# Kernel optimization log

Measured on AMD Instinct MI355X. Metric: run time of the kernel, lower is better.

The kernel has to match this reference:

```python
import jax, jax.numpy as jnp
import numpy as np

K_CENTERS = 128   # SA K
RADIUS = 1.0      # SA r
D = 3             # spatial dim (module-level d)
IFD = 64          # input feature dim
L1, L2, L3 = 64, 64, 128
N_POINTS = 8192


def setup_inputs() -> dict:
    key = jax.random.key(0)
    ks = jax.random.split(key, 8)
    coords = jax.random.normal(ks[0], (N_POINTS, D), dtype=jnp.float32)
    features = jax.random.normal(ks[1], (N_POINTS, IFD), dtype=jnp.float32)

    def lin(kw, kb, fan_in, fan_out):
        bound = 1.0 / np.sqrt(fan_in)
        W = jax.random.uniform(kw, (fan_in, fan_out), jnp.float32, -bound, bound)
        b = jax.random.uniform(kb, (fan_out,), jnp.float32, -bound, bound)
        return W, b

    W1, b1 = lin(ks[2], ks[3], D + IFD, L1)
    W2, b2 = lin(ks[4], ks[5], L1, L2)
    W3, b3 = lin(ks[6], ks[7], L2, L3)
    return dict(coords=coords, features=features,
                W1=W1, b1=b1, W2=W2, b2=b2, W3=W3, b3=b3)


def farthest_point_sample(coords, k):
    """Iterative FPS starting from point 0 (pytorch3d default). Returns [k] indices."""
    n = coords.shape[0]

    def step(carry, _):
        dists, last = carry
        d2 = jnp.sum((coords - coords[last]) ** 2, axis=1)  # [N]
        dists = jnp.minimum(dists, d2)
        nxt = jnp.argmax(dists).astype(jnp.int32)
        return (dists, nxt), nxt

    init = (jnp.full((n,), 1e10, coords.dtype), jnp.int32(0))
    (_, _), rest = jax.lax.scan(step, init, None, length=k - 1)
    return jnp.concatenate([jnp.zeros((1,), jnp.int32), rest])


def reference(coords, features, W1, b1, W2, b2, W3, b3):
    # 1) Farthest point sampling -> K centers
    idx = farthest_point_sample(coords, K_CENTERS)
    centers = coords[idx]                                  # [K, 3]

    # 2) Ball-query grouping (mask form): point p in group(c) iff ||p - c|| < r.
    rel = coords[None, :, :] - centers[:, None, :]         # [K, N, 3] (coords - center)
    mask = jnp.linalg.norm(rel, axis=-1) < RADIUS          # [K, N]

    # 3) Per-group PointNet: shared MLP on [rel_coords, features], then masked max over group.
    feat = jnp.broadcast_to(features[None, :, :], (K_CENTERS,) + features.shape)
    x = jnp.concatenate([rel, feat], axis=-1)              # [K, N, 3+ifd]
    h = jax.nn.relu(x @ W1 + b1)                           # [K, N, l1]
    h = jax.nn.relu(h @ W2 + b2)                           # [K, N, l2]
    h = jax.nn.relu(h @ W3 + b3)                           # [K, N, l3]
    h = jnp.where(mask[..., None], h, -jnp.inf)            # exclude out-of-ball points
    out_features = jnp.max(h, axis=1)                      # [K, l3]
    return centers, out_features
```

## Files before the change

kernel.cpp:

```cpp
#include <hip/hip_runtime.h>

#define N_POINTS 8192
#define K_CENTERS 128
#define IFD 64
#define L1D 64
#define L2D 64
#define L3D 128
#define QS 4096

#define LD4(p) (*(const float4*)(p))

template <int CTRL, int RMASK>
__device__ __forceinline__ void dpp_max_u64(unsigned& hi, unsigned& lo) {
  unsigned h2 = (unsigned)__builtin_amdgcn_update_dpp(
      (int)hi, (int)hi, CTRL, RMASK, 0xF, false);
  unsigned l2 = (unsigned)__builtin_amdgcn_update_dpp(
      (int)lo, (int)lo, CTRL, RMASK, 0xF, false);
  unsigned long long a = ((unsigned long long)hi << 32) | lo;
  unsigned long long b = ((unsigned long long)h2 << 32) | l2;
  if (b > a) { hi = h2; lo = l2; }
}

#define FPS_T 512
#define FPS_P (N_POINTS / FPS_T)

#define SMEM_BYTES (98304 + 128)

__global__ __launch_bounds__(FPS_T) void fps_gt_kernel(
    const float* __restrict__ coords, float* __restrict__ out_centers,
    const float* __restrict__ features, const float* __restrict__ W1,
    const float* __restrict__ b1, float* __restrict__ GT,
    int* __restrict__ counts, float* __restrict__ out_feat) {
  __shared__ __align__(16) char smem[SMEM_BYTES];
  const int tid = threadIdx.x;

  if (blockIdx.x != 0) {
    float* w = (float*)smem;
    const int bk = blockIdx.x - 1;
    if (bk == 0 && tid < K_CENTERS) counts[tid] = 0;
    if (bk == 1) {
#pragma unroll 1
      for (int s = tid; s < K_CENTERS * L3D; s += FPS_T) out_feat[s] = 0.0f;
    }
    const int n0 = bk * 64;
    for (int s = tid; s < IFD * L1D; s += FPS_T) w[s] = W1[3 * L1D + s];
    __syncthreads();
    const int j = tid & 63;
    const int nl = tid >> 6;
    const float bj = b1[j];
#pragma unroll 1
    for (int itn = 0; itn < 8; itn++) {
      const int nn = nl + itn * 8;
      const float* __restrict__ frow = features + (size_t)(n0 + nn) * IFD;
      float acc = bj;
#pragma unroll 16
      for (int i = 0; i < IFD; i++) acc = fmaf(frow[i], w[i * 64 + j], acc);
      GT[(size_t)(n0 + nn) * 64 + j] = acc;
    }
    return;
  }

  float* clds = (float*)smem;
  unsigned long long* wmax = (unsigned long long*)(smem + 98304);
  const int lane = tid & 63;
  const int wid = tid >> 6;

  {
    const float4* __restrict__ src = (const float4*)coords;
    float4* dst = (float4*)smem;
#pragma unroll
    for (int i = 0; i < 12; i++) dst[tid + i * FPS_T] = src[tid + i * FPS_T];
  }

  float px[FPS_P], py[FPS_P], pz[FPS_P], mind[FPS_P];
#pragma unroll
  for (int i = 0; i < FPS_P; i++) {
    int n = tid + i * FPS_T;
    px[i] = coords[3 * n];
    py[i] = coords[3 * n + 1];
    pz[i] = coords[3 * n + 2];
    mind[i] = 1e10f;
  }

  float cx = coords[0], cy = coords[1], cz = coords[2];
  if (tid == 0) {
    out_centers[0] = cx; out_centers[1] = cy; out_centers[2] = cz;
  }
  __syncthreads();

  for (int it = 1; it < K_CENTERS; it++) {
#pragma unroll
    for (int i = 0; i < FPS_P; i++) {
      float dx = px[i] - cx, dy = py[i] - cy, dz = pz[i] - cz;
      float d2 = dx * dx + dy * dy + dz * dz;
      mind[i] = fminf(mind[i], d2);
    }
    float t8[8];
#pragma unroll
    for (int i = 0; i < 8; i++) t8[i] = fmaxf(mind[i], mind[i + 8]);
#pragma unroll
    for (int i = 0; i < 4; i++) t8[i] = fmaxf(t8[i], t8[i + 4]);
    const float bm = fmaxf(fmaxf(t8[0], t8[1]), fmaxf(t8[2], t8[3]));
    int cand[FPS_P];
#pragma unroll
    for (int i = 0; i < FPS_P; i++)
      cand[i] = (mind[i] == bm) ? (tid + i * FPS_T) : 0x7FFFFFFF;
#pragma unroll
    for (int s = 8; s > 0; s >>= 1)
#pragma unroll
      for (int i = 0; i < s; i++) cand[i] = min(cand[i], cand[i + s]);

    unsigned hi = __float_as_uint(bm);
    unsigned lo = (unsigned)(N_POINTS - 1 - cand[0]);
    dpp_max_u64<0xB1, 0xF>(hi, lo);
    dpp_max_u64<0x4E, 0xF>(hi, lo);
    dpp_max_u64<0x141, 0xF>(hi, lo);
    dpp_max_u64<0x140, 0xF>(hi, lo);
    dpp_max_u64<0x142, 0xA>(hi, lo);
    dpp_max_u64<0x143, 0xC>(hi, lo);
    const int buf = it & 1;
    if (lane == 63)
      wmax[(buf << 3) + wid] = ((unsigned long long)hi << 32) | lo;
    __syncthreads();

    const unsigned long long* __restrict__ wb = wmax + (buf << 3);
    unsigned long long a0 = wb[0], a1 = wb[1], a2 = wb[2], a3 = wb[3];
    unsigned long long a4 = wb[4], a5 = wb[5], a6 = wb[6], a7 = wb[7];
    a0 = a0 > a4 ? a0 : a4;
    a1 = a1 > a5 ? a1 : a5;
    a2 = a2 > a6 ? a2 : a6;
    a3 = a3 > a7 ? a3 : a7;
    a0 = a0 > a2 ? a0 : a2;
    a1 = a1 > a3 ? a1 : a3;
    a0 = a0 > a1 ? a0 : a1;
    const int widx = N_POINTS - 1 - (int)(a0 & 0xFFFFFFFFull);
    cx = clds[widx * 3];
    cy = clds[widx * 3 + 1];
    cz = clds[widx * 3 + 2];
    if (tid == 0) {
      out_centers[3 * it] = cx;
      out_centers[3 * it + 1] = cy;
      out_centers[3 * it + 2] = cz;
    }
  }
}

#define PREP_PARTS 4
#define PREP_PTS (N_POINTS / PREP_PARTS)

__global__ __launch_bounds__(256) void prep_kernel(
    const float* __restrict__ coords, const float* __restrict__ centers,
    int* __restrict__ counts, int* __restrict__ Q) {
  const int tid = threadIdx.x;
  const int k = blockIdx.x >> 2;
  const int part = blockIdx.x & 3;
  const float cx = centers[3 * k], cy = centers[3 * k + 1],
              cz = centers[3 * k + 2];
  const int nbase = part * PREP_PTS;
#pragma unroll
  for (int s = 0; s < PREP_PTS / 256; s++) {
    const int n = nbase + s * 256 + tid;
    float dx = coords[3 * n] - cx;
    float dy = coords[3 * n + 1] - cy;
    float dz = coords[3 * n + 2] - cz;
    float d2 = dx * dx + dy * dy + dz * dz;
    if (sqrtf(d2) < 1.0f) {
      int p = atomicAdd(&counts[k], 1);
      if (p < QS) Q[(k << 12) + p] = n;
    }
  }
}

#define MLP_BLOCKS 1024

__global__ __launch_bounds__(256, 4) void mlp_kernel(
    const float* __restrict__ coords, const float* __restrict__ GT,
    const float* __restrict__ W1, const float* __restrict__ W2,
    const float* __restrict__ b2, const float* __restrict__ W3,
    const float* __restrict__ b3, const float* __restrict__ centers,
    const int* __restrict__ counts, const int* __restrict__ Q,
    float* __restrict__ out_feat) {
  __shared__ float gt2[64 * 65];
  __shared__ float cst[3 * 64 + 64 + 128];
  const int tid = threadIdx.x;
  const int lane = tid & 63;
  const int wid = tid >> 6;
  const int gu = __builtin_amdgcn_readfirstlane(wid);

  for (int s = tid; s < 384; s += 256) {
    float v;
    if (s < 192) v = W1[s];
    else if (s < 256) v = b2[s - 192];
    else v = b3[s - 256];
    cst[s] = v;
  }

  int c0c = counts[lane];      if (c0c > QS) c0c = QS;
  int c1c = counts[64 + lane]; if (c1c > QS) c1c = QS;
  int s0 = (c0c + 63) >> 6;
  int s1 = (c1c + 63) >> 6;
#pragma unroll
  for (int off = 1; off < 64; off <<= 1) {
    int t0 = __shfl_up(s0, off, 64);
    int t1 = __shfl_up(s1, off, 64);
    if (lane >= off) { s0 += t0; s1 += t1; }
  }
  s1 += __shfl(s0, 63, 64);
  const int C = __shfl(s1, 63, 64);
  const int p1 = s0;
  const int p65 = s1;

  const int cpb = (C + MLP_BLOCKS - 1) / MLP_BLOCKS;
  const int cbeg = blockIdx.x * cpb;
  const int cend = min(cbeg + cpb, C);
  __syncthreads();
  if (cbeg >= C) return;

  float vmax[32];
#pragma unroll
  for (int t = 0; t < 32; t++) vmax[t] = 0.0f;
  int kprev = -1;

  for (int c = cbeg; c < cend; c++) {
    int k = __popcll(__ballot(p1 <= c)) + __popcll(__ballot(p65 <= c));
    k = __builtin_amdgcn_readfirstlane(k);
    int pk = 0;
    if (k > 0)
      pk = (k <= 64) ? __shfl(s0, k - 1, 64) : __shfl(s1, k - 65, 64);
    int Mk = counts[k];
    if (Mk > QS) Mk = QS;
    const int m0 = (c - pk) * 64;
    const int base = (k << 12) + m0;
    const int mcap = Mk - 1 - m0;

    if (k != kprev) {
      if (kprev >= 0) {
#pragma unroll
        for (int t = 0; t < 32; t++) {
          float v = vmax[t];
#pragma unroll
          for (int off = 32; off >= 1; off >>= 1)
            v = fmaxf(v, __shfl_xor(v, off, 64));
          if (lane == 0)
            atomicMax((unsigned int*)&out_feat[kprev * L3D + gu * 32 + t],
                      __float_as_uint(v));
          vmax[t] = 0.0f;
        }
      }
      kprev = k;
    }

#pragma unroll 4
    for (int it = 0; it < 16; it++) {
      int row = (gu << 4) + it;
      int rr = row < mcap ? row : mcap;
      int nrow = Q[base + rr];
      nrow = __builtin_amdgcn_readfirstlane(nrow);
      gt2[row * 65 + lane] = GT[(size_t)nrow * 64 + lane];
    }
    __syncthreads();

    int m = m0 + lane;
    if (m >= Mk) m = Mk - 1;
    const int n = Q[(k << 12) + m];
    const float cx = centers[3 * k], cy = centers[3 * k + 1],
                cz = centers[3 * k + 2];
    const float dx = coords[3 * n] - cx;
    const float dy = coords[3 * n + 1] - cy;
    const float dz = coords[3 * n + 2] - cz;

    float acc[16];
#pragma unroll
    for (int t = 0; t < 16; t++) acc[t] = cst[192 + gu * 16 + t];
    const float* __restrict__ w2u = W2 + gu * 16;
#pragma unroll 4
    for (int i = 0; i < 64; i++) {
      const float g = gt2[lane * 65 + i];
      const float e = fmaxf(
          fmaf(dz, cst[128 + i], fmaf(dy, cst[64 + i], fmaf(dx, cst[i], g))),
          0.0f);
      const float* __restrict__ wr = w2u + i * 64;
#pragma unroll
      for (int t = 0; t < 16; t += 4) {
        const float4 w = LD4(wr + t);
        acc[t + 0] = fmaf(e, w.x, acc[t + 0]);
        acc[t + 1] = fmaf(e, w.y, acc[t + 1]);
        acc[t + 2] = fmaf(e, w.z, acc[t + 2]);
        acc[t + 3] = fmaf(e, w.w, acc[t + 3]);
      }
    }
    __syncthreads();

#pragma unroll
    for (int t = 0; t < 16; t++)
      gt2[lane * 65 + gu * 16 + t] = fmaxf(acc[t], 0.0f);
    __syncthreads();

    float a3[32];
#pragma unroll
    for (int t = 0; t < 32; t++) a3[t] = cst[256 + gu * 32 + t];
    const float* __restrict__ w3u = W3 + gu * 32;
#pragma unroll 2
    for (int i = 0; i < 64; i++) {
      const float hv = gt2[lane * 65 + i];
      const float* __restrict__ wr = w3u + i * L3D;
#pragma unroll
      for (int t = 0; t < 32; t += 4) {
        const float4 w = LD4(wr + t);
        a3[t + 0] = fmaf(hv, w.x, a3[t + 0]);
        a3[t + 1] = fmaf(hv, w.y, a3[t + 1]);
        a3[t + 2] = fmaf(hv, w.z, a3[t + 2]);
        a3[t + 3] = fmaf(hv, w.w, a3[t + 3]);
      }
    }
#pragma unroll
    for (int t = 0; t < 32; t++)
      vmax[t] = fmaxf(vmax[t], fmaxf(a3[t], 0.0f));
    __syncthreads();
  }

#pragma unroll
  for (int t = 0; t < 32; t++) {
    float v = vmax[t];
#pragma unroll
    for (int off = 32; off >= 1; off >>= 1)
      v = fmaxf(v, __shfl_xor(v, off, 64));
    if (lane == 0)
      atomicMax((unsigned int*)&out_feat[kprev * L3D + gu * 32 + t],
                __float_as_uint(v));
  }
}

extern "C" void kernel_launch(void* const* d_in, const int* in_sizes, int n_in,
                              void* d_out, int out_size, void* d_ws,
                              size_t ws_size, hipStream_t stream) {
  const float* coords = (const float*)d_in[0];
  const float* features = (const float*)d_in[1];
  const float* W1 = (const float*)d_in[2];
  const float* b1 = (const float*)d_in[3];
  const float* W2 = (const float*)d_in[4];
  const float* b2 = (const float*)d_in[5];
  const float* W3 = (const float*)d_in[6];
  const float* b3 = (const float*)d_in[7];

  float* out = (float*)d_out;
  float* centers = out;
  float* out_feat = out + K_CENTERS * 3;

  char* ws = (char*)d_ws;
  float* GT = (float*)ws;
  int* Q = (int*)(ws + (size_t)N_POINTS * L1D * 4);
  int* counts = (int*)(ws + 4 * 1024 * 1024);

  fps_gt_kernel<<<1 + K_CENTERS, FPS_T, 0, stream>>>(
      coords, centers, features, W1, b1, GT, counts, out_feat);
  prep_kernel<<<PREP_PARTS * K_CENTERS, 256, 0, stream>>>(coords, centers,
                                                          counts, Q);
  mlp_kernel<<<MLP_BLOCKS, 256, 0, stream>>>(coords, GT, W1, W2, b2, W3, b3,
                                             centers, counts, Q, out_feat);
}
```

Before: 236.3 us.

## Fuse FPS, ball query and MLP into one persistent kernel with flag-based streaming

Merges the three kernels into one persistent launch. Block 0 runs farthest point sampling and publishes each center through a progress counter. The other 160 worker blocks first compute the GT projection, then take (center, slice) tickets and do the ball query and MLP for each center as soon as it is published. This overlaps the serial FPS with the grouping and MLP work and removes the global queue and extra launches. Weights are staged in LDS. The design depends on all blocks being co-resident and on spin-waiting, and the workers may simply stall behind the sequential FPS chain.

```diff
diff --git a/kernel.cpp b/kernel.cpp
--- a/kernel.cpp
+++ b/kernel.cpp
@@ -6,7 +6,6 @@
 #define L1D 64
 #define L2D 64
 #define L3D 128
-#define QS 4096
 
 #define LD4(p) (*(const float4*)(p))
 
@@ -23,311 +22,322 @@
 
 #define FPS_T 512
 #define FPS_P (N_POINTS / FPS_T)
-
 #define SMEM_BYTES (98304 + 128)
 
-__global__ __launch_bounds__(FPS_T) void fps_gt_kernel(
+#define NWORK 160
+#define GT_ROWS 52
+#define SLICES 8
+#define SLICE_PTS (N_POINTS / SLICES)
+#define TICKETS (K_CENTERS * SLICES)
+
+__global__ void zero_ctrl(int* __restrict__ ctrl) {
+  if (threadIdx.x < 8) ctrl[threadIdx.x] = 0;
+}
+
+__global__ __launch_bounds__(512) void fused_kernel(
     const float* __restrict__ coords, float* __restrict__ out_centers,
     const float* __restrict__ features, const float* __restrict__ W1,
-    const float* __restrict__ b1, float* __restrict__ GT,
-    int* __restrict__ counts, float* __restrict__ out_feat) {
+    const float* __restrict__ b1, const float* __restrict__ W2,
+    const float* __restrict__ b2, const float* __restrict__ W3,
+    const float* __restrict__ b3, float* __restrict__ GT,
+    int* __restrict__ ctrl, unsigned* __restrict__ cbuf,
+    float* __restrict__ out_feat) {
   __shared__ __align__(16) char smem[SMEM_BYTES];
-  const int tid = threadIdx.x;
-
-  if (blockIdx.x != 0) {
-    float* w = (float*)smem;
-    const int bk = blockIdx.x - 1;
-    if (bk == 0 && tid < K_CENTERS) counts[tid] = 0;
-    if (bk == 1) {
-#pragma unroll 1
-      for (int s = tid; s < K_CENTERS * L3D; s += FPS_T) out_feat[s] = 0.0f;
-    }
-    const int n0 = bk * 64;
-    for (int s = tid; s < IFD * L1D; s += FPS_T) w[s] = W1[3 * L1D + s];
-    __syncthreads();
-    const int j = tid & 63;
-    const int nl = tid >> 6;
-    const float bj = b1[j];
-#pragma unroll 1
-    for (int itn = 0; itn < 8; itn++) {
-      const int nn = nl + itn * 8;
-      const float* __restrict__ frow = features + (size_t)(n0 + nn) * IFD;
-      float acc = bj;
-#pragma unroll 16
-      for (int i = 0; i < IFD; i++) acc = fmaf(frow[i], w[i * 64 + j], acc);
-      GT[(size_t)(n0 + nn) * 64 + j] = acc;
-    }
-    return;
-  }
-
-  float* clds = (float*)smem;
-  unsigned long long* wmax = (unsigned long long*)(smem + 98304);
-  const int lane = tid & 63;
-  const int wid = tid >> 6;
-
-  {
-    const float4* __restrict__ src = (const float4*)coords;
-    float4* dst = (float4*)smem;
-#pragma unroll
-    for (int i = 0; i < 12; i++) dst[tid + i * FPS_T] = src[tid + i * FPS_T];
-  }
-
-  float px[FPS_P], py[FPS_P], pz[FPS_P], mind[FPS_P];
-#pragma unroll
-  for (int i = 0; i < FPS_P; i++) {
-    int n = tid + i * FPS_T;
-    px[i] = coords[3 * n];
-    py[i] = coords[3 * n + 1];
-    pz[i] = coords[3 * n + 2];
-    mind[i] = 1e10f;
-  }
-
-  float cx = coords[0], cy = coords[1], cz = coords[2];
-  if (tid == 0) {
-    out_centers[0] = cx; out_centers[1] = cy; out_centers[2] = cz;
-  }
-  __syncthreads();
-
-  for (int it = 1; it < K_CENTERS; it++) {
-#pragma unroll
-    for (int i = 0; i < FPS_P; i++) {
-      float dx = px[i] - cx, dy = py[i] - cy, dz = pz[i] - cz;
-      float d2 = dx * dx + dy * dy + dz * dz;
-      mind[i] = fminf(mind[i], d2);
-    }
-    float t8[8];
-#pragma unroll
-    for (int i = 0; i < 8; i++) t8[i] = fmaxf(mind[i], mind[i + 8]);
-#pragma unroll
-    for (int i = 0; i < 4; i++) t8[i] = fmaxf(t8[i], t8[i + 4]);
-    const float bm = fmaxf(fmaxf(t8[0], t8[1]), fmaxf(t8[2], t8[3]));
-    int cand[FPS_P];
-#pragma unroll
-    for (int i = 0; i < FPS_P; i++)
-      cand[i] = (mind[i] == bm) ? (tid + i * FPS_T) : 0x7FFFFFFF;
-#pragma unroll
-    for (int s = 8; s > 0; s >>= 1)
-#pragma unroll
-      for (int i = 0; i < s; i++) cand[i] = min(cand[i], cand[i + s]);
-
-    unsigned hi = __float_as_uint(bm);
-    unsigned lo = (unsigned)(N_POINTS - 1 - cand[0]);
-    dpp_max_u64<0xB1, 0xF>(hi, lo);
-    dpp_max_u64<0x4E, 0xF>(hi, lo);
-    dpp_max_u64<0x141, 0xF>(hi, lo);
-    dpp_max_u64<0x140, 0xF>(hi, lo);
-    dpp_max_u64<0x142, 0xA>(hi, lo);
-    dpp_max_u64<0x143, 0xC>(hi, lo);
-    const int buf = it & 1;
-    if (lane == 63)
-      wmax[(buf << 3) + wid] = ((unsigned long long)hi << 32) | lo;
-    __syncthreads();
-
-    const unsigned long long* __restrict__ wb = wmax + (buf << 3);
-    unsigned long long a0 = wb[0], a1 = wb[1], a2 = wb[2], a3 = wb[3];
-    unsigned long long a4 = wb[4], a5 = wb[5], a6 = wb[6], a7 = wb[7];
-    a0 = a0 > a4 ? a0 : a4;
-    a1 = a1 > a5 ? a1 : a5;
-    a2 = a2 > a6 ? a2 : a6;
-    a3 = a3 > a7 ? a3 : a7;
-    a0 = a0 > a2 ? a0 : a2;
-    a1 = a1 > a3 ? a1 : a3;
-    a0 = a0 > a1 ? a0 : a1;
-    const int widx = N_POINTS - 1 - (int)(a0 & 0xFFFFFFFFull);
-    cx = clds[widx * 3];
-    cy = clds[widx * 3 + 1];
-    cz = clds[widx * 3 + 2];
-    if (tid == 0) {
-      out_centers[3 * it] = cx;
-      out_centers[3 * it + 1] = cy;
-      out_centers[3 * it + 2] = cz;
-    }
-  }
-}
-
-#define PREP_PARTS 4
-#define PREP_PTS (N_POINTS / PREP_PARTS)
-
-__global__ __launch_bounds__(256) void prep_kernel(
-    const float* __restrict__ coords, const float* __restrict__ centers,
-    int* __restrict__ counts, int* __restrict__ Q) {
-  const int tid = threadIdx.x;
-  const int k = blockIdx.x >> 2;
-  const int part = blockIdx.x & 3;
-  const float cx = centers[3 * k], cy = centers[3 * k + 1],
-              cz = centers[3 * k + 2];
-  const int nbase = part * PREP_PTS;
-#pragma unroll
-  for (int s = 0; s < PREP_PTS / 256; s++) {
-    const int n = nbase + s * 256 + tid;
-    float dx = coords[3 * n] - cx;
-    float dy = coords[3 * n + 1] - cy;
-    float dz = coords[3 * n + 2] - cz;
-    float d2 = dx * dx + dy * dy + dz * dz;
-    if (sqrtf(d2) < 1.0f) {
-      int p = atomicAdd(&counts[k], 1);
-      if (p < QS) Q[(k << 12) + p] = n;
-    }
-  }
-}
-
-#define MLP_BLOCKS 1024
-
-__global__ __launch_bounds__(256, 4) void mlp_kernel(
-    const float* __restrict__ coords, const float* __restrict__ GT,
-    const float* __restrict__ W1, const float* __restrict__ W2,
-    const float* __restrict__ b2, const float* __restrict__ W3,
-    const float* __restrict__ b3, const float* __restrict__ centers,
-    const int* __restrict__ counts, const int* __restrict__ Q,
-    float* __restrict__ out_feat) {
-  __shared__ float gt2[64 * 65];
-  __shared__ float cst[3 * 64 + 64 + 128];
   const int tid = threadIdx.x;
   const int lane = tid & 63;
   const int wid = tid >> 6;
-  const int gu = __builtin_amdgcn_readfirstlane(wid);
-
-  for (int s = tid; s < 384; s += 256) {
-    float v;
-    if (s < 192) v = W1[s];
-    else if (s < 256) v = b2[s - 192];
-    else v = b3[s - 256];
-    cst[s] = v;
-  }
-
-  int c0c = counts[lane];      if (c0c > QS) c0c = QS;
-  int c1c = counts[64 + lane]; if (c1c > QS) c1c = QS;
-  int s0 = (c0c + 63) >> 6;
-  int s1 = (c1c + 63) >> 6;
-#pragma unroll
-  for (int off = 1; off < 64; off <<= 1) {
-    int t0 = __shfl_up(s0, off, 64);
-    int t1 = __shfl_up(s1, off, 64);
-    if (lane >= off) { s0 += t0; s1 += t1; }
-  }
-  s1 += __shfl(s0, 63, 64);
-  const int C = __shfl(s1, 63, 64);
-  const int p1 = s0;
-  const int p65 = s1;
-
-  const int cpb = (C + MLP_BLOCKS - 1) / MLP_BLOCKS;
-  const int cbeg = blockIdx.x * cpb;
-  const int cend = min(cbeg + cpb, C);
+
+  int* prog = ctrl + 0;
+  int* gt_done = ctrl + 1;
+  int* ticket = ctrl + 2;
+
+  if (blockIdx.x == 0) {
+    float* clds = (float*)smem;
+    unsigned long long* wmax = (unsigned long long*)(smem + 98304);
+
+    {
+      const float4* __restrict__ src = (const float4*)coords;
+      float4* dst = (float4*)smem;
+#pragma unroll
+      for (int i = 0; i < 12; i++)
+        dst[tid + i * FPS_T] = src[tid + i * FPS_T];
+    }
+
+    float px[FPS_P], py[FPS_P], pz[FPS_P], mind[FPS_P];
+#pragma unroll
+    for (int i = 0; i < FPS_P; i++) {
+      int n = tid + i * FPS_T;
+      px[i] = coords[3 * n];
+      py[i] = coords[3 * n + 1];
+      pz[i] = coords[3 * n + 2];
+      mind[i] = 1e10f;
+    }
+
+    float cx = coords[0], cy = coords[1], cz = coords[2];
+    if (tid == 0) {
+      out_centers[0] = cx; out_centers[1] = cy; out_centers[2] = cz;
+      __hip_atomic_store(&cbuf[0], __float_as_uint(cx), __ATOMIC_RELAXED,
+                         __HIP_MEMORY_SCOPE_AGENT);
+      __hip_atomic_store(&cbuf[1], __float_as_uint(cy), __ATOMIC_RELAXED,
+                         __HIP_MEMORY_SCOPE_AGENT);
+      __hip_atomic_store(&cbuf[2], __float_as_uint(cz), __ATOMIC_RELAXED,
+                         __HIP_MEMORY_SCOPE_AGENT);
+      __hip_atomic_store(prog, 1, __ATOMIC_RELEASE, __HIP_MEMORY_SCOPE_AGENT);
+    }
+    __syncthreads();
+
+    for (int it = 1; it < K_CENTERS; it++) {
+#pragma unroll
+      for (int i = 0; i < FPS_P; i++) {
+        float dx = px[i] - cx, dy = py[i] - cy, dz = pz[i] - cz;
+        float d2 = dx * dx + dy * dy + dz * dz;
+        mind[i] = fminf(mind[i], d2);
+      }
+      float t8[8];
+#pragma unroll
+      for (int i = 0; i < 8; i++) t8[i] = fmaxf(mind[i], mind[i + 8]);
+#pragma unroll
+      for (int i = 0; i < 4; i++) t8[i] = fmaxf(t8[i], t8[i + 4]);
+      const float bm = fmaxf(fmaxf(t8[0], t8[1]), fmaxf(t8[2], t8[3]));
+      int cand[FPS_P];
+#pragma unroll
+      for (int i = 0; i < FPS_P; i++)
+        cand[i] = (mind[i] == bm) ? (tid + i * FPS_T) : 0x7FFFFFFF;
+#pragma unroll
+      for (int s = 8; s > 0; s >>= 1)
+#pragma unroll
+        for (int i = 0; i < s; i++) cand[i] = min(cand[i], cand[i + s]);
+
+      unsigned hi = __float_as_uint(bm);
+      unsigned lo = (unsigned)(N_POINTS - 1 - cand[0]);
+      dpp_max_u64<0xB1, 0xF>(hi, lo);
+      dpp_max_u64<0x4E, 0xF>(hi, lo);
+      dpp_max_u64<0x141, 0xF>(hi, lo);
+      dpp_max_u64<0x140, 0xF>(hi, lo);
+      dpp_max_u64<0x142, 0xA>(hi, lo);
+      dpp_max_u64<0x143, 0xC>(hi, lo);
+      const int buf = it & 1;
+      if (lane == 63)
+        wmax[(buf << 3) + wid] = ((unsigned long long)hi << 32) | lo;
+      __syncthreads();
+
+      const unsigned long long* __restrict__ wb = wmax + (buf << 3);
+      unsigned long long a0 = wb[0], a1 = wb[1], a2 = wb[2], a3 = wb[3];
+      unsigned long long a4 = wb[4], a5 = wb[5], a6 = wb[6], a7 = wb[7];
+      a0 = a0 > a4 ? a0 : a4;
+      a1 = a1 > a5 ? a1 : a5;
+      a2 = a2 > a6 ? a2 : a6;
+      a3 = a3 > a7 ? a3 : a7;
+      a0 = a0 > a2 ? a0 : a2;
+      a1 = a1 > a3 ? a1 : a3;
+      a0 = a0 > a1 ? a0 : a1;
+      const int widx = N_POINTS - 1 - (int)(a0 & 0xFFFFFFFFull);
+      cx = clds[widx * 3];
+      cy = clds[widx * 3 + 1];
+      cz = clds[widx * 3 + 2];
+      if (tid == 0) {
+        out_centers[3 * it] = cx;
+        out_centers[3 * it + 1] = cy;
+        out_centers[3 * it + 2] = cz;
+        __hip_atomic_store(&cbuf[3 * it], __float_as_uint(cx),
+                           __ATOMIC_RELAXED, __HIP_MEMORY_SCOPE_AGENT);
+        __hip_atomic_store(&cbuf[3 * it + 1], __float_as_uint(cy),
+                           __ATOMIC_RELAXED, __HIP_MEMORY_SCOPE_AGENT);
+        __hip_atomic_store(&cbuf[3 * it + 2], __float_as_uint(cz),
+                           __ATOMIC_RELAXED, __HIP_MEMORY_SCOPE_AGENT);
+        __hip_atomic_store(prog, it + 1, __ATOMIC_RELEASE,
+                           __HIP_MEMORY_SCOPE_AGENT);
+      }
+    }
+    return;
+  }
+
+  float* w2s = (float*)smem;
+  float* w3s = (float*)(smem + 16384);
+  float* gt2 = (float*)(smem + 49152);
+  float* cst = (float*)(smem + 65792);
+  int* q = (int*)(smem + 67328);
+  int* bc = (int*)(smem + 71424);
+
+  const int wb = blockIdx.x - 1;
+
+  for (int s = tid; s < IFD * L1D; s += 512) w2s[s] = W1[3 * L1D + s];
   __syncthreads();
-  if (cbeg >= C) return;
-
-  float vmax[32];
-#pragma unroll
-  for (int t = 0; t < 32; t++) vmax[t] = 0.0f;
-  int kprev = -1;
-
-  for (int c = cbeg; c < cend; c++) {
-    int k = __popcll(__ballot(p1 <= c)) + __popcll(__ballot(p65 <= c));
-    k = __builtin_amdgcn_readfirstlane(k);
-    int pk = 0;
-    if (k > 0)
-      pk = (k <= 64) ? __shfl(s0, k - 1, 64) : __shfl(s1, k - 65, 64);
-    int Mk = counts[k];
-    if (Mk > QS) Mk = QS;
-    const int m0 = (c - pk) * 64;
-    const int base = (k << 12) + m0;
-    const int mcap = Mk - 1 - m0;
-
-    if (k != kprev) {
-      if (kprev >= 0) {
-#pragma unroll
-        for (int t = 0; t < 32; t++) {
-          float v = vmax[t];
-#pragma unroll
-          for (int off = 32; off >= 1; off >>= 1)
-            v = fmaxf(v, __shfl_xor(v, off, 64));
-          if (lane == 0)
-            atomicMax((unsigned int*)&out_feat[kprev * L3D + gu * 32 + t],
-                      __float_as_uint(v));
-          vmax[t] = 0.0f;
+  {
+    const int r0 = wb * GT_ROWS;
+    const int r1 = min(r0 + GT_ROWS, N_POINTS);
+    const float bj = b1[lane];
+    for (int r = r0 + wid; r < r1; r += 8) {
+      const float* __restrict__ frow = features + (size_t)r * IFD;
+      float acc = bj;
+#pragma unroll 16
+      for (int i = 0; i < IFD; i++)
+        acc = fmaf(frow[i], w2s[i * 64 + lane], acc);
+      __hip_atomic_store(&GT[(size_t)r * 64 + lane], acc, __ATOMIC_RELAXED,
+                         __HIP_MEMORY_SCOPE_AGENT);
+    }
+  }
+  if (wb < 32) {
+    __hip_atomic_store(&out_feat[wb * 512 + tid], 0.0f, __ATOMIC_RELAXED,
+                       __HIP_MEMORY_SCOPE_AGENT);
+  }
+  __threadfence();
+  __syncthreads();
+  if (tid == 0) atomicAdd(gt_done, 1);
+
+  for (int s = tid; s < 64 * 64; s += 512) w2s[s] = W2[s];
+  for (int s = tid; s < 64 * 128; s += 512) w3s[s] = W3[s];
+  if (tid < 384) {
+    float v = (tid < 192) ? W1[tid]
+                          : (tid < 256 ? b2[tid - 192] : b3[tid - 256]);
+    cst[tid] = v;
+  }
+  if (tid == 0) {
+    while (__hip_atomic_load(gt_done, __ATOMIC_ACQUIRE,
+                             __HIP_MEMORY_SCOPE_AGENT) < NWORK)
+      __builtin_amdgcn_s_sleep(2);
+  }
+  __syncthreads();
+
+  for (;;) {
+    if (tid == 0) bc[0] = atomicAdd(ticket, 1);
+    __syncthreads();
+    const int t = bc[0];
+    if (t >= TICKETS) break;
+    const int k = t >> 3;
+    const int slice = t & 7;
+
+    if (tid == 0) {
+      while (__hip_atomic_load(prog, __ATOMIC_ACQUIRE,
+                               __HIP_MEMORY_SCOPE_AGENT) < k + 1)
+        __builtin_amdgcn_s_sleep(2);
+      bc[1] = (int)__hip_atomic_load(&cbuf[3 * k], __ATOMIC_RELAXED,
+                                     __HIP_MEMORY_SCOPE_AGENT);
+      bc[2] = (int)__hip_atomic_load(&cbuf[3 * k + 1], __ATOMIC_RELAXED,
+                                     __HIP_MEMORY_SCOPE_AGENT);
+      bc[3] = (int)__hip_atomic_load(&cbuf[3 * k + 2], __ATOMIC_RELAXED,
+                                     __HIP_MEMORY_SCOPE_AGENT);
+      bc[4] = 0;
+    }
+    __syncthreads();
+    const float ckx = __uint_as_float((unsigned)bc[1]);
+    const float cky = __uint_as_float((unsigned)bc[2]);
+    const float ckz = __uint_as_float((unsigned)bc[3]);
+
+    const int nb = slice * SLICE_PTS;
+#pragma unroll
+    for (int it2 = 0; it2 < SLICE_PTS / 512; it2++) {
+      const int n = nb + it2 * 512 + tid;
+      const float ddx = coords[3 * n] - ckx;
+      const float ddy = coords[3 * n + 1] - cky;
+      const float ddz = coords[3 * n + 2] - ckz;
+      const float d2 = ddx * ddx + ddy * ddy + ddz * ddz;
+      if (sqrtf(d2) < 1.0f) {
+        int p = atomicAdd(&bc[4], 1);
+        q[p] = n;
+      }
+    }
+    __syncthreads();
+    const int M = bc[4];
+
+    if (M > 0) {
+      const int nc = (M + 63) >> 6;
+      float vmax[16];
+#pragma unroll
+      for (int t2 = 0; t2 < 16; t2++) vmax[t2] = 0.0f;
+
+      for (int c = 0; c < nc; c++) {
+        const int m0 = c << 6;
+#pragma unroll
+        for (int jr = 0; jr < 8; jr++) {
+          const int row = (wid << 3) + jr;
+          int mm = m0 + row;
+          if (mm >= M) mm = M - 1;
+          int nrow = q[mm];
+          nrow = __builtin_amdgcn_readfirstlane(nrow);
+          gt2[row * 65 + lane] = GT[(size_t)nrow * 64 + lane];
         }
-      }
-      kprev = k;
-    }
-
+        __syncthreads();
+
+        int m = m0 + lane;
+        if (m >= M) m = M - 1;
+        const int n = q[m];
+        const float dx = coords[3 * n] - ckx;
+        const float dy = coords[3 * n + 1] - cky;
+        const float dz = coords[3 * n + 2] - ckz;
+
+        float acc[8];
+#pragma unroll
+        for (int t2 = 0; t2 < 8; t2++) acc[t2] = cst[192 + (wid << 3) + t2];
 #pragma unroll 4
-    for (int it = 0; it < 16; it++) {
-      int row = (gu << 4) + it;
-      int rr = row < mcap ? row : mcap;
-      int nrow = Q[base + rr];
-      nrow = __builtin_amdgcn_readfirstlane(nrow);
-      gt2[row * 65 + lane] = GT[(size_t)nrow * 64 + lane];
-    }
-    __syncthreads();
-
-    int m = m0 + lane;
-    if (m >= Mk) m = Mk - 1;
-    const int n = Q[(k << 12) + m];
-    const float cx = centers[3 * k], cy = centers[3 * k + 1],
-                cz = centers[3 * k + 2];
-    const float dx = coords[3 * n] - cx;
-    const float dy = coords[3 * n + 1] - cy;
-    const float dz = coords[3 * n + 2] - cz;
-
-    float acc[16];
-#pragma unroll
-    for (int t = 0; t < 16; t++) acc[t] = cst[192 + gu * 16 + t];
-    const float* __restrict__ w2u = W2 + gu * 16;
-#pragma unroll 4
-    for (int i = 0; i < 64; i++) {
-      const float g = gt2[lane * 65 + i];
-      const float e = fmaxf(
-          fmaf(dz, cst[128 + i], fmaf(dy, cst[64 + i], fmaf(dx, cst[i], g))),
-          0.0f);
-      const float* __restrict__ wr = w2u + i * 64;
-#pragma unroll
-      for (int t = 0; t < 16; t += 4) {
-        const float4 w = LD4(wr + t);
-        acc[t + 0] = fmaf(e, w.x, acc[t + 0]);
-        acc[t + 1] = fmaf(e, w.y, acc[t + 1]);
-        acc[t + 2] = fmaf(e, w.z, acc[t + 2]);
-        acc[t + 3] = fmaf(e, w.w, acc[t + 3]);
-      }
-    }
-    __syncthreads();
-
-#pragma unroll
-    for (int t = 0; t < 16; t++)
-      gt2[lane * 65 + gu * 16 + t] = fmaxf(acc[t], 0.0f);
-    __syncthreads();
-
-    float a3[32];
-#pragma unroll
-    for (int t = 0; t < 32; t++) a3[t] = cst[256 + gu * 32 + t];
-    const float* __restrict__ w3u = W3 + gu * 32;
+        for (int i = 0; i < 64; i++) {
+          const float g = gt2[lane * 65 + i];
+          const float e = fmaxf(
+              fmaf(dz, cst[128 + i],
+                   fmaf(dy, cst[64 + i], fmaf(dx, cst[i], g))),
+              0.0f);
+          const float4 wa = LD4(w2s + i * 64 + (wid << 3));
+          const float4 wb4 = LD4(w2s + i * 64 + (wid << 3) + 4);
+          acc[0] = fmaf(e, wa.x, acc[0]);
+          acc[1] = fmaf(e, wa.y, acc[1]);
+          acc[2] = fmaf(e, wa.z, acc[2]);
+          acc[3] = fmaf(e, wa.w, acc[3]);
+          acc[4] = fmaf(e, wb4.x, acc[4]);
+          acc[5] = fmaf(e, wb4.y, acc[5]);
+          acc[6] = fmaf(e, wb4.z, acc[6]);
+          acc[7] = fmaf(e, wb4.w, acc[7]);
+        }
+        __syncthreads();
+#pragma unroll
+        for (int t2 = 0; t2 < 8; t2++)
+          gt2[lane * 65 + (wid << 3) + t2] = fmaxf(acc[t2], 0.0f);
+        __syncthreads();
+
+        float a3[16];
+#pragma unroll
+        for (int t2 = 0; t2 < 16; t2++) a3[t2] = cst[256 + (wid << 4) + t2];
 #pragma unroll 2
-    for (int i = 0; i < 64; i++) {
-      const float hv = gt2[lane * 65 + i];
-      const float* __restrict__ wr = w3u + i * L3D;
-#pragma unroll
-      for (int t = 0; t < 32; t += 4) {
-        const float4 w = LD4(wr + t);
-        a3[t + 0] = fmaf(hv, w.x, a3[t + 0]);
-        a3[t + 1] = fmaf(hv, w.y, a3[t + 1]);
-        a3[t + 2] = fmaf(hv, w.z, a3[t + 2]);
-        a3[t + 3] = fmaf(hv, w.w, a3[t + 3]);
-      }
-    }
-#pragma unroll
-    for (int t = 0; t < 32; t++)
-      vmax[t] = fmaxf(vmax[t], fmaxf(a3[t], 0.0f));
-    __syncthreads();
-  }
-
-#pragma unroll
-  for (int t = 0; t < 32; t++) {
-    float v = vmax[t];
-#pragma unroll
-    for (int off = 32; off >= 1; off >>= 1)
-      v = fmaxf(v, __shfl_xor(v, off, 64));
-    if (lane == 0)
-      atomicMax((unsigned int*)&out_feat[kprev * L3D + gu * 32 + t],
-                __float_as_uint(v));
+        for (int i = 0; i < 64; i++) {
+          const float hv = gt2[lane * 65 + i];
+          const float* __restrict__ w3r = w3s + i * L3D + (wid << 4);
+          const float4 wa = LD4(w3r);
+          const float4 wb4 = LD4(w3r + 4);
+          const float4 wc = LD4(w3r + 8);
+          const float4 wd = LD4(w3r + 12);
+          a3[0] = fmaf(hv, wa.x, a3[0]);
+          a3[1] = fmaf(hv, wa.y, a3[1]);
+          a3[2] = fmaf(hv, wa.z, a3[2]);
+          a3[3] = fmaf(hv, wa.w, a3[3]);
+          a3[4] = fmaf(hv, wb4.x, a3[4]);
+          a3[5] = fmaf(hv, wb4.y, a3[5]);
+          a3[6] = fmaf(hv, wb4.z, a3[6]);
+          a3[7] = fmaf(hv, wb4.w, a3[7]);
+          a3[8] = fmaf(hv, wc.x, a3[8]);
+          a3[9] = fmaf(hv, wc.y, a3[9]);
+          a3[10] = fmaf(hv, wc.z, a3[10]);
+          a3[11] = fmaf(hv, wc.w, a3[11]);
+          a3[12] = fmaf(hv, wd.x, a3[12]);
+          a3[13] = fmaf(hv, wd.y, a3[13]);
+          a3[14] = fmaf(hv, wd.z, a3[14]);
+          a3[15] = fmaf(hv, wd.w, a3[15]);
+        }
+#pragma unroll
+        for (int t2 = 0; t2 < 16; t2++)
+          vmax[t2] = fmaxf(vmax[t2], fmaxf(a3[t2], 0.0f));
+        __syncthreads();
+      }
+
+#pragma unroll
+      for (int t2 = 0; t2 < 16; t2++) {
+        float v = vmax[t2];
+#pragma unroll
+        for (int off = 32; off >= 1; off >>= 1)
+          v = fmaxf(v, __shfl_xor(v, off, 64));
+        if (lane == 0)
+          atomicMax((unsigned*)&out_feat[k * L3D + (wid << 4) + t2],
+                    __float_as_uint(v));
+      }
+    }
   }
 }
 
@@ -349,13 +359,11 @@
 
   char* ws = (char*)d_ws;
   float* GT = (float*)ws;
-  int* Q = (int*)(ws + (size_t)N_POINTS * L1D * 4);
-  int* counts = (int*)(ws + 4 * 1024 * 1024);
-
-  fps_gt_kernel<<<1 + K_CENTERS, FPS_T, 0, stream>>>(
-      coords, centers, features, W1, b1, GT, counts, out_feat);
-  prep_kernel<<<PREP_PARTS * K_CENTERS, 256, 0, stream>>>(coords, centers,
-                                                          counts, Q);
-  mlp_kernel<<<MLP_BLOCKS, 256, 0, stream>>>(coords, GT, W1, W2, b2, W3, b3,
-                                             centers, counts, Q, out_feat);
+  int* ctrl = (int*)(ws + (size_t)N_POINTS * L1D * 4);
+  unsigned* cbuf = (unsigned*)(ws + (size_t)N_POINTS * L1D * 4 + 64);
+
+  zero_ctrl<<<1, 64, 0, stream>>>(ctrl);
+  fused_kernel<<<1 + NWORK, 512, 0, stream>>>(coords, centers, features, W1,
+                                              b1, W2, b2, W3, b3, GT, ctrl,
+                                              cbuf, out_feat);
 }
```

After: 258.5 us. 9.4% more time.
